# Optimization experiments

Measured on AMD Instinct MI355X. Metric: run time of the kernel, lower is better.

Reference implementation:

```python
import jax, jax.numpy as jnp
import numpy as np

FEAT_STRIDE = 16
PRE_NMS = 6000   # TEST config
POST_NMS = 300
NMS_TH = 0.7


def _generate_anchors_3d(base_size=16, ratios=(0.5, 1.0, 2.0), scales=(8, 16, 32), time_dims=(16,)):
    """Standard Faster-RCNN anchor enumeration, extended with a time extent.
    Returns (A, 6) float32 boxes in [x1, y1, z1, x2, y2, z2] order (matches shift order)."""
    w = h = float(base_size)
    xc = yc = 0.5 * (base_size - 1)
    size = w * h
    ratios = np.asarray(ratios, dtype=np.float64)
    ws = np.round(np.sqrt(size / ratios))
    hs = np.round(ws * ratios)
    a2 = []
    for wi, hi in zip(ws, hs):
        for s in scales:
            ww, hh = wi * s, hi * s
            a2.append([xc - 0.5 * (ww - 1), yc - 0.5 * (hh - 1),
                       xc + 0.5 * (ww - 1), yc + 0.5 * (hh - 1)])
    out = []
    for t in time_dims:
        for a in a2:
            out.append([a[0], a[1], 0.0, a[2], a[3], float(t) - 1.0])
    return np.asarray(out, dtype=np.float32)


def setup_inputs() -> dict:
    key = jax.random.key(0)
    k1, k2 = jax.random.split(key)
    B, A, H, W, T = 2, 9, 32, 32, 16
    scores_map = jax.random.normal(k1, (B, 2 * A, H, W, T), dtype=jnp.float32)
    bbox_frame = jax.random.normal(k2, (B, 6 * A, H, W, T), dtype=jnp.float32) * 0.2
    im_info = jnp.array([512.0, 512.0, 16.0], dtype=jnp.float32)  # [img_h, img_w, n_frames]
    anchors = jnp.asarray(_generate_anchors_3d())  # (9, 6)
    return {"scores_map": scores_map, "bbox_frame": bbox_frame, "im_info": im_info, "anchors": anchors}


def _nms_single(boxes, scs):
    """Greedy 3D (spatio-temporal volume) NMS for one image.
    boxes: (N, 6), scs: (N,). Returns (POST_NMS, 7) rows [score, x1,y1,z1,x2,y2,z2],
    zero-padded past the number of kept proposals (matches output[i].zero_() + fill)."""
    order = jnp.argsort(-scs)[:PRE_NMS]           # descending score, pre-NMS top-k
    b = boxes[order]                              # (P, 6)
    s = scs[order]                                # (P,)
    vol = (b[:, 3] - b[:, 0] + 1.0) * (b[:, 4] - b[:, 1] + 1.0) * (b[:, 5] - b[:, 2] + 1.0)
    iw = jnp.clip(jnp.minimum(b[:, None, 3], b[None, :, 3]) - jnp.maximum(b[:, None, 0], b[None, :, 0]) + 1.0, 0.0)
    ih = jnp.clip(jnp.minimum(b[:, None, 4], b[None, :, 4]) - jnp.maximum(b[:, None, 1], b[None, :, 1]) + 1.0, 0.0)
    il = jnp.clip(jnp.minimum(b[:, None, 5], b[None, :, 5]) - jnp.maximum(b[:, None, 2], b[None, :, 2]) + 1.0, 0.0)
    inter = iw * ih * il                          # (P, P)
    iou = inter / (vol[:, None] + vol[None, :] - inter)
    iou = jax.lax.stop_gradient(iou)              # keep mask is non-differentiable
    P = b.shape[0]
    idx = jnp.arange(P)

    def step(keep, i):
        sup = (iou[i] > NMS_TH) & keep[i] & (idx > i)
        return keep & ~sup, None

    keep, _ = jax.lax.scan(step, jnp.ones((P,), dtype=bool), jnp.arange(P))
    rank = jnp.cumsum(keep) - 1
    pos = jnp.where(keep & (rank < POST_NMS), rank, POST_NMS)  # overflow slot POST_NMS
    rows = jnp.concatenate([s[:, None], b], axis=1)            # (P, 7)
    out = jnp.zeros((POST_NMS + 1, 7), dtype=boxes.dtype).at[pos].set(rows)
    return out[:POST_NMS]


def reference(scores_map, bbox_frame, im_info, anchors):
    A = anchors.shape[0]
    B = scores_map.shape[0]
    scores = scores_map[:, A:]                    # (B, A, H, W, T) foreground scores
    H, W, T = scores.shape[2], scores.shape[3], scores.shape[4]

    # --- anchor grid (matches np.meshgrid 'xy' + ravel = H-major, W, T order) ---
    sx = (jnp.arange(W) * FEAT_STRIDE).astype(scores_map.dtype)
    sy = (jnp.arange(H) * FEAT_STRIDE).astype(scores_map.dtype)
    sz = jnp.arange(T).astype(scores_map.dtype)
    X, Y, Z = jnp.meshgrid(sx, sy, sz)            # each (H, W, T)
    shift = jnp.stack([X.ravel(), Y.ravel(), Z.ravel()], axis=1)   # (K, 3)
    shifts = jnp.concatenate([shift, shift], axis=1)               # (K, 6)
    all_anchors = (anchors[None] + shifts[:, None]).reshape(-1, 6)  # (K*A, 6)

    deltas = bbox_frame.transpose(0, 2, 3, 4, 1).reshape(B, -1, 6)  # (B, K*A, 6)
    scs = scores.transpose(0, 2, 3, 4, 1).reshape(B, -1)            # (B, K*A)

    # --- bbox_transform_inv_3d ---
    aw = all_anchors[:, 3] - all_anchors[:, 0] + 1.0
    ah = all_anchors[:, 4] - all_anchors[:, 1] + 1.0
    al = all_anchors[:, 5] - all_anchors[:, 2] + 1.0
    acx = all_anchors[:, 0] + 0.5 * aw
    acy = all_anchors[:, 1] + 0.5 * ah
    acz = all_anchors[:, 2] + 0.5 * al
    pcx = deltas[..., 0] * aw + acx
    pcy = deltas[..., 1] * ah + acy
    pcz = deltas[..., 2] * al + acz
    pw = jnp.exp(deltas[..., 3]) * aw
    ph = jnp.exp(deltas[..., 4]) * ah
    pl = jnp.exp(deltas[..., 5]) * al
    proposals = jnp.stack([pcx - 0.5 * pw, pcy - 0.5 * ph, pcz - 0.5 * pl,
                           pcx + 0.5 * pw, pcy + 0.5 * ph, pcz + 0.5 * pl], axis=-1)

    # --- clip_boxes_3d: x in [0, img_w-1], y in [0, img_h-1], z in [0, n_frames-1] ---
    lim = jnp.stack([im_info[1], im_info[0], im_info[2],
                     im_info[1], im_info[0], im_info[2]]) - 1.0
    proposals = jnp.clip(proposals, 0.0, lim)

    return jax.vmap(_nms_single)(proposals, scs)  # (B, POST_NMS, 7)
```

## Files before the change

### kernel.cpp

```cpp
#include <hip/hip_runtime.h>
#include <stdint.h>

#define FEAT_STRIDE 16
#define PRE_NMS 6000
#define POST_NMS 300
#define NMS_TH 0.7f

static constexpr int B_ = 2, A_ = 9, H_ = 32, W_ = 32, T_ = 16;
static constexpr int LOC = H_ * W_ * T_;
static constexpr int N_ = LOC * A_;
static constexpr int NBIN = 65536;
static constexpr int NREP = 8;
static constexpr int CAP = 8192;
static constexpr int NW = 94;
static constexpr int ROWS = 6016;


__device__ __forceinline__ uint32_t f2u(float f) {
    uint32_t b = __float_as_uint(f);
    return b ^ ((b >> 31) ? 0xFFFFFFFFu : 0x80000000u);
}
__device__ __forceinline__ float u2f(uint32_t u) {
    uint32_t b = (u >> 31) ? (u ^ 0x80000000u) : ~u;
    return __uint_as_float(b);
}

__global__ void hist_kernel(const float* __restrict__ scores_map,
                            unsigned int* __restrict__ histR) {
    int gid = blockIdx.x * blockDim.x + threadIdx.x;
    if (gid >= B_ * N_) return;
    int b = gid / N_;
    int r = gid - b * N_;
    int a = r / LOC;
    int loc = r - a * LOC;
    float sc = scores_map[((size_t)(b * 2 * A_ + A_ + a)) * LOC + loc];
    uint32_t u = f2u(sc);
    int rep = blockIdx.x & (NREP - 1);
    atomicAdd(&histR[((size_t)(rep * B_ + b)) * NBIN + (u >> 16)], 1u);
}

__global__ void __launch_bounds__(256) partial_kernel(
        const unsigned int* __restrict__ histR,
        unsigned int* __restrict__ partials) {
    int c = blockIdx.x, bb = blockIdx.y, t = threadIdx.x;
    unsigned int s = 0;
#pragma unroll
    for (int r = 0; r < NREP; ++r) {
        const uint4* h4 = reinterpret_cast<const uint4*>(
            histR + ((size_t)(r * B_ + bb)) * NBIN + c * 1024);
        uint4 v = h4[t];
        s += v.x + v.y + v.z + v.w;
    }
    __shared__ unsigned int red[256];
    red[t] = s;
    __syncthreads();
    for (int off = 128; off > 0; off >>= 1) {
        if (t < off) red[t] += red[t + off];
        __syncthreads();
    }
    if (t == 0) partials[bb * 64 + c] = red[0];
}

__global__ void __launch_bounds__(256) rewrite_kernel(
        const unsigned int* __restrict__ histR,
        unsigned int* __restrict__ hist,
        unsigned int* __restrict__ binbase,
        const unsigned int* __restrict__ partials,
        unsigned int* __restrict__ thr) {
    int c = blockIdx.x, bb = blockIdx.y, t = threadIdx.x;
    __shared__ unsigned int sp[64];
    __shared__ unsigned int ssum[256];
    if (t < 64) sp[t] = partials[bb * 64 + t];
    uint4 v = {0u, 0u, 0u, 0u};
#pragma unroll
    for (int r = 0; r < NREP; ++r) {
        const uint4* h4 = reinterpret_cast<const uint4*>(
            histR + ((size_t)(r * B_ + bb)) * NBIN + c * 1024);
        uint4 w = h4[t];
        v.x += w.x; v.y += w.y; v.z += w.z; v.w += w.w;
    }
    unsigned int* h = hist + (size_t)bb * NBIN + c * 1024;
    unsigned int* bs = binbase + (size_t)bb * NBIN + c * 1024;
    ssum[t] = v.x + v.y + v.z + v.w;
    __syncthreads();
    unsigned int chunkBase = 0;
    for (int q = c + 1; q < 64; ++q) chunkBase += sp[q];
    for (int off = 1; off < 256; off <<= 1) {
        unsigned int val = (t + off < 256) ? ssum[t + off] : 0u;
        __syncthreads();
        ssum[t] += val;
        __syncthreads();
    }
    unsigned int run = chunkBase + ((t < 255) ? ssum[t + 1] : 0u);
    unsigned int cnt[4] = {v.x, v.y, v.z, v.w};
    unsigned int offv[4];
    for (int q = 3; q >= 0; --q) {
        offv[q] = run;
        unsigned int newrun = run + cnt[q];
        if (run < (unsigned)PRE_NMS && newrun >= (unsigned)PRE_NMS) {
            thr[bb * 2 + 0] = (unsigned)(c * 1024 + t * 4 + q);
            thr[bb * 2 + 1] = newrun;
        }
        run = newrun;
    }
    uint4 o4 = {offv[0], offv[1], offv[2], offv[3]};
    reinterpret_cast<uint4*>(h)[t] = o4;
    reinterpret_cast<uint4*>(bs)[t] = o4;
}

__global__ void __launch_bounds__(256) compact_kernel(
        const float* __restrict__ scores_map,
        const unsigned int* __restrict__ thr,
        unsigned long long* __restrict__ cand,
        unsigned int* __restrict__ hist) {
    int tid = threadIdx.x;
    int gid = blockIdx.x * 256 + tid;
    int b = gid / N_;
    int r = gid - b * N_;
    int a = r / LOC;
    int loc = r - a * LOC;
    float sc = scores_map[((size_t)(b * 2 * A_ + A_ + a)) * LOC + loc];
    uint32_t u = f2u(sc);
    uint32_t bin = u >> 16;
    if (bin >= thr[b * 2]) {
        int n = loc * A_ + a;
        unsigned long long key = ((unsigned long long)u << 18)
                               | (unsigned long long)(N_ - 1 - n);
        unsigned int slot = atomicAdd(&hist[b * NBIN + bin], 1u);
        if (slot < (unsigned)CAP)
            cand[(size_t)b * CAP + slot] = key;
    }
}

__global__ void __launch_bounds__(256) bucket_decode(
        const unsigned long long* __restrict__ cand,
        const unsigned int* __restrict__ hist,
        const unsigned int* __restrict__ binbase,
        const unsigned int* __restrict__ thr,
        const float* __restrict__ bbox_frame,
        const float* __restrict__ im_info,
        const float* __restrict__ anchors,
        float* __restrict__ sortedBox) {
    int gid = blockIdx.x * 256 + threadIdx.x;
    int bb = gid / CAP;
    int i = gid - bb * CAP;
    int count = (int)thr[bb * 2 + 1];
    if (count > CAP) count = CAP;
    if (i >= count) return;
    const unsigned long long* cb = cand + (size_t)bb * CAP;
    unsigned long long me = cb[i];
    int bin = (int)(me >> 34);
    int start = (int)binbase[bb * NBIN + bin];
    int end = (int)hist[bb * NBIN + bin];
    if (end > count) end = count;
    int rank = start;
    for (int q = start; q < end; ++q)
        rank += (cb[q] > me);
    if (rank >= PRE_NMS) return;

    uint32_t u = (uint32_t)(me >> 18);
    int n = N_ - 1 - (int)(me & 0x3FFFFull);
    int a = n % A_;
    int loc = n / A_;
    int k = loc % T_;
    int j = (loc / T_) % W_;
    int ii = loc / (T_ * W_);

    float ax1 = anchors[a * 6 + 0] + (float)(FEAT_STRIDE * j);
    float ay1 = anchors[a * 6 + 1] + (float)(FEAT_STRIDE * ii);
    float az1 = anchors[a * 6 + 2] + (float)k;
    float ax2 = anchors[a * 6 + 3] + (float)(FEAT_STRIDE * j);
    float ay2 = anchors[a * 6 + 4] + (float)(FEAT_STRIDE * ii);
    float az2 = anchors[a * 6 + 5] + (float)k;
    float aw = ax2 - ax1 + 1.0f, ah = ay2 - ay1 + 1.0f, al = az2 - az1 + 1.0f;
    float acx = ax1 + 0.5f * aw, acy = ay1 + 0.5f * ah, acz = az1 + 0.5f * al;

    const float* dp = bbox_frame + ((size_t)(bb * 6 * A_ + a * 6)) * LOC
                    + ii * (W_ * T_) + j * T_ + k;
    float d0 = dp[0 * LOC], d1 = dp[1 * LOC], d2 = dp[2 * LOC];
    float d3 = dp[3 * LOC], d4 = dp[4 * LOC], d5 = dp[5 * LOC];

    float pcx = d0 * aw + acx, pcy = d1 * ah + acy, pcz = d2 * al + acz;
    float pw = expf(d3) * aw, ph = expf(d4) * ah, pl = expf(d5) * al;

    float x1 = pcx - 0.5f * pw, y1 = pcy - 0.5f * ph, z1 = pcz - 0.5f * pl;
    float x2 = pcx + 0.5f * pw, y2 = pcy + 0.5f * ph, z2 = pcz + 0.5f * pl;

    float lx = im_info[1] - 1.0f, ly = im_info[0] - 1.0f, lz = im_info[2] - 1.0f;
    x1 = fminf(fmaxf(x1, 0.0f), lx); y1 = fminf(fmaxf(y1, 0.0f), ly); z1 = fminf(fmaxf(z1, 0.0f), lz);
    x2 = fminf(fmaxf(x2, 0.0f), lx); y2 = fminf(fmaxf(y2, 0.0f), ly); z2 = fminf(fmaxf(z2, 0.0f), lz);

    float vol = (x2 - x1 + 1.0f) * (y2 - y1 + 1.0f) * (z2 - z1 + 1.0f);
    float* p = sortedBox + ((size_t)bb * ROWS + rank) * 8;
    p[0] = x1; p[1] = y1; p[2] = z1; p[3] = x2;
    p[4] = y2; p[5] = z2; p[6] = vol; p[7] = u2f(u);
}

__global__ void mask_build(const float* __restrict__ sortedBox,
                           unsigned long long* __restrict__ mask,
                           unsigned long long* __restrict__ diagBand) {
    int g = blockIdx.x / NW, w = blockIdx.x % NW;
    if (w < g) return;
    int bb = blockIdx.y;
    int lane = threadIdx.x;
    __shared__ float colb[64][7];
    const float* sb = sortedBox + (size_t)bb * ROWS * 8;
    int col = w * 64 + lane;
    if (col < PRE_NMS) {
        const float4* cp4 = reinterpret_cast<const float4*>(sb + (size_t)col * 8);
        float4 lo = cp4[0], hi = cp4[1];
        colb[lane][0] = lo.x; colb[lane][1] = lo.y; colb[lane][2] = lo.z;
        colb[lane][3] = lo.w; colb[lane][4] = hi.x; colb[lane][5] = hi.y;
        colb[lane][6] = hi.z;
    } else {
        colb[lane][0] = 3e8f; colb[lane][1] = 0.f; colb[lane][2] = 0.f;
        colb[lane][3] = -3e8f; colb[lane][4] = 0.f; colb[lane][5] = 0.f;
        colb[lane][6] = 1.0f;
    }
    __syncthreads();
    int row = g * 64 + lane;
    if (row >= PRE_NMS) return;
    const float4* rp4 = reinterpret_cast<const float4*>(sb + (size_t)row * 8);
    float4 rlo = rp4[0], rhi = rp4[1];
    float x1 = rlo.x, y1 = rlo.y, z1 = rlo.z;
    float x2 = rlo.w, y2 = rhi.x, z2 = rhi.y, v = rhi.z;
    unsigned long long word = 0;
    for (int b2 = 0; b2 < 64; ++b2) {
        float iw = fminf(x2, colb[b2][3]) - fmaxf(x1, colb[b2][0]) + 1.0f;
        float ih = fminf(y2, colb[b2][4]) - fmaxf(y1, colb[b2][1]) + 1.0f;
        float il = fminf(z2, colb[b2][5]) - fmaxf(z1, colb[b2][2]) + 1.0f;
        iw = fmaxf(iw, 0.0f); ih = fmaxf(ih, 0.0f); il = fmaxf(il, 0.0f);
        float inter = iw * ih * il;
        float iou = inter / (v + colb[b2][6] - inter);
        int cidx = w * 64 + b2;
        if (cidx > row && iou > NMS_TH) word |= (1ull << b2);
    }
    mask[((size_t)bb * ROWS + row) * NW + w] = word;
    if (w == g) {
        diagBand[((size_t)bb * ROWS + row) * 2 + 0] = word;
        if (g == NW - 1) diagBand[((size_t)bb * ROWS + row) * 2 + 1] = 0ull;
    }
    if (w == g + 1) diagBand[((size_t)bb * ROWS + row) * 2 + 1] = word;
}

__global__ void __launch_bounds__(1024) suppress_kernel(
        const unsigned long long* __restrict__ mask,
        const unsigned long long* __restrict__ diagBand,
        const float* __restrict__ sortedBox,
        float* __restrict__ out) {
    int bb = blockIdx.x;
    int tid = threadIdx.x;
    int lane = tid & 63;
    __shared__ unsigned long long remv[NW];
    __shared__ int kr[2][64];
    __shared__ int s_nk;
    for (int i = tid; i < NW; i += 1024) remv[i] = 0ull;
    if (tid == 0) {
        remv[NW - 1] = ~((1ull << (PRE_NMS - (NW - 1) * 64)) - 1ull);
        s_nk = 0;
    }
    __syncthreads();

    const unsigned long long* M = mask + (size_t)bb * ROWS * NW;
    const unsigned long long* D = diagBand + (size_t)bb * ROWS * 2;
    const float* sb = sortedBox + (size_t)bb * ROWS * 8;
    float* ob = out + (size_t)bb * POST_NMS * 7;

    int kept_total = 0, prev_nk = 0, prev_base = 0, cur = 0;
    unsigned long long diag0 = 0, band1 = 0, sup = 0;
    if (tid < 64) {
        diag0 = D[lane * 2 + 0];
        band1 = D[lane * 2 + 1];
    }

    for (int c = 0; c < NW; ++c) {
        unsigned long long nxt0 = 0, nxt1 = 0;
        if (tid < 64) {
            if (c + 1 < NW) {
                nxt0 = D[((c + 1) * 64 + lane) * 2 + 0];
                nxt1 = D[((c + 1) * 64 + lane) * 2 + 1];
            }
            unsigned long long alive = ~(remv[c] | sup);
            unsigned long long supn = 0;
            int nk = 0;
            while (alive && kept_total + nk < POST_NMS) {
                int b = __builtin_ctzll(alive);
                if (lane == 0) kr[cur][nk] = c * 64 + b;
                ++nk;
                alive &= ~(__shfl(diag0, b) | (1ull << b));
                supn |= __shfl(band1, b);
            }
            sup = supn;
            if (tid == 0) s_nk = nk;
        } else {
            int t = tid - 64;
            for (int w2 = c + 1 + t; w2 < NW; w2 += 960) {
                unsigned long long v = remv[w2];
                for (int i = 0; i < prev_nk; ++i)
                    v |= M[(size_t)kr[cur ^ 1][i] * NW + w2];
                remv[w2] = v;
            }
            for (int e = t; e < prev_nk * 7; e += 960) {
                int i = e / 7, j = e - i * 7;
                ob[(size_t)(prev_base + i) * 7 + j] =
                    sb[(size_t)kr[cur ^ 1][i] * 8 + (j == 0 ? 7 : j - 1)];
            }
        }
        __syncthreads();
        int nk = s_nk;
        prev_base = kept_total;
        kept_total += nk;
        prev_nk = nk;
        cur ^= 1;
        if (tid < 64) { diag0 = nxt0; band1 = nxt1; }
        if (kept_total >= POST_NMS) break;
    }
    for (int e = tid; e < prev_nk * 7; e += 1024) {
        int i = e / 7, j = e - i * 7;
        ob[(size_t)(prev_base + i) * 7 + j] =
            sb[(size_t)kr[cur ^ 1][i] * 8 + (j == 0 ? 7 : j - 1)];
    }
    for (int idx = kept_total * 7 + tid; idx < POST_NMS * 7; idx += 1024)
        ob[idx] = 0.0f;
}

extern "C" void kernel_launch(void* const* d_in, const int* in_sizes, int n_in,
                              void* d_out, int out_size, void* d_ws, size_t ws_size,
                              hipStream_t stream) {
    const float* scores_map = (const float*)d_in[0];
    const float* bbox_frame = (const float*)d_in[1];
    const float* im_info    = (const float*)d_in[2];
    const float* anchors    = (const float*)d_in[3];
    float* out = (float*)d_out;

    char* ws = (char*)d_ws;
    unsigned long long* mask     = (unsigned long long*)(ws + 0);
    unsigned int* binbase        = (unsigned int*)(ws + 0);
    unsigned int* histR          = (unsigned int*)(ws + 524288);
    float* sortedBox             = (float*)(ws + 9048064);
    unsigned long long* cand     = (unsigned long long*)(ws + 9433088);
    unsigned int* hist           = (unsigned int*)(ws + 9564160);
    unsigned long long* diagBand = (unsigned long long*)(ws + 9564160);
    unsigned int* thr            = (unsigned int*)(ws + 10088448);
    unsigned int* partials       = (unsigned int*)(ws + 10088464);

    hipMemsetAsync(histR, 0, (size_t)NREP * B_ * NBIN * 4, stream);

    int total = B_ * N_;
    hist_kernel<<<(total + 255) / 256, 256, 0, stream>>>(scores_map, histR);
    partial_kernel<<<dim3(64, B_), 256, 0, stream>>>(histR, partials);
    rewrite_kernel<<<dim3(64, B_), 256, 0, stream>>>(histR, hist, binbase, partials, thr);
    compact_kernel<<<total / 256, 256, 0, stream>>>(scores_map, thr, cand, hist);
    bucket_decode<<<B_ * CAP / 256, 256, 0, stream>>>(cand, hist, binbase, thr,
                                                      bbox_frame, im_info, anchors,
                                                      sortedBox);
    mask_build<<<dim3(NW * NW, B_), 64, 0, stream>>>(sortedBox, mask, diagBand);
    suppress_kernel<<<B_, 1024, 0, stream>>>(mask, diagBand, sortedBox, out);
}
```

Baseline: 144.3 us.

## Replace IoU division with double-precision compare, vectorize shared column loads, transpose mask

The per-pair IoU division in mask building is replaced by a multiply-compare in double against a constant chosen to reproduce the float `iou > 0.7` decision. Column boxes are staged in shared memory as two float4 arrays so each inner iteration does vector LDS reads, and the loop is unrolled. The suppression mask is stored word-major instead of row-major, so the suppress kernel reads one mask word's rows at contiguous addresses. Double-precision arithmetic may be slower on some paths, and the exactness of the threshold equivalence depends on the chosen constant.

New measurement: 134.1 us. 1.08x faster.

```diff
diff --git a/kernel.cpp b/kernel.cpp
--- a/kernel.cpp
+++ b/kernel.cpp
@@ -14,6 +14,8 @@
 static constexpr int CAP = 8192;
 static constexpr int NW = 94;
 static constexpr int ROWS = 6016;
+
+static constexpr double BMID = 0.7000000178813934326171875;
 
 
 __device__ __forceinline__ uint32_t f2u(float f) {
@@ -203,19 +205,18 @@
     if (w < g) return;
     int bb = blockIdx.y;
     int lane = threadIdx.x;
-    __shared__ float colb[64][7];
+    __shared__ float4 colA[64];
+    __shared__ float4 colB[64];
     const float* sb = sortedBox + (size_t)bb * ROWS * 8;
     int col = w * 64 + lane;
     if (col < PRE_NMS) {
         const float4* cp4 = reinterpret_cast<const float4*>(sb + (size_t)col * 8);
         float4 lo = cp4[0], hi = cp4[1];
-        colb[lane][0] = lo.x; colb[lane][1] = lo.y; colb[lane][2] = lo.z;
-        colb[lane][3] = lo.w; colb[lane][4] = hi.x; colb[lane][5] = hi.y;
-        colb[lane][6] = hi.z;
+        colA[lane] = make_float4(lo.x, lo.y, lo.z, lo.w);
+        colB[lane] = make_float4(hi.x, hi.y, hi.z, 0.0f);
     } else {
-        colb[lane][0] = 3e8f; colb[lane][1] = 0.f; colb[lane][2] = 0.f;
-        colb[lane][3] = -3e8f; colb[lane][4] = 0.f; colb[lane][5] = 0.f;
-        colb[lane][6] = 1.0f;
+        colA[lane] = make_float4(3e8f, 0.0f, 0.0f, -3e8f);
+        colB[lane] = make_float4(0.0f, 0.0f, 1.0f, 0.0f);
     }
     __syncthreads();
     int row = g * 64 + lane;
@@ -225,17 +226,21 @@
     float x1 = rlo.x, y1 = rlo.y, z1 = rlo.z;
     float x2 = rlo.w, y2 = rhi.x, z2 = rhi.y, v = rhi.z;
     unsigned long long word = 0;
+#pragma unroll 8
     for (int b2 = 0; b2 < 64; ++b2) {
-        float iw = fminf(x2, colb[b2][3]) - fmaxf(x1, colb[b2][0]) + 1.0f;
-        float ih = fminf(y2, colb[b2][4]) - fmaxf(y1, colb[b2][1]) + 1.0f;
-        float il = fminf(z2, colb[b2][5]) - fmaxf(z1, colb[b2][2]) + 1.0f;
+        float4 cA = colA[b2];
+        float4 cB = colB[b2];
+        float iw = fminf(x2, cA.w) - fmaxf(x1, cA.x) + 1.0f;
+        float ih = fminf(y2, cB.x) - fmaxf(y1, cA.y) + 1.0f;
+        float il = fminf(z2, cB.y) - fmaxf(z1, cA.z) + 1.0f;
         iw = fmaxf(iw, 0.0f); ih = fmaxf(ih, 0.0f); il = fmaxf(il, 0.0f);
         float inter = iw * ih * il;
-        float iou = inter / (v + colb[b2][6] - inter);
+        float denom = v + cB.z - inter;
+        bool over = ((double)inter >= BMID * (double)denom);
         int cidx = w * 64 + b2;
-        if (cidx > row && iou > NMS_TH) word |= (1ull << b2);
-    }
-    mask[((size_t)bb * ROWS + row) * NW + w] = word;
+        if (cidx > row && over) word |= (1ull << b2);
+    }
+    mask[((size_t)bb * NW + w) * ROWS + row] = word;
     if (w == g) {
         diagBand[((size_t)bb * ROWS + row) * 2 + 0] = word;
         if (g == NW - 1) diagBand[((size_t)bb * ROWS + row) * 2 + 1] = 0ull;
@@ -261,7 +266,7 @@
     }
     __syncthreads();
 
-    const unsigned long long* M = mask + (size_t)bb * ROWS * NW;
+    const unsigned long long* M = mask + (size_t)bb * NW * ROWS;
     const unsigned long long* D = diagBand + (size_t)bb * ROWS * 2;
     const float* sb = sortedBox + (size_t)bb * ROWS * 8;
     float* ob = out + (size_t)bb * POST_NMS * 7;
@@ -295,10 +300,10 @@
         } else {
             int t = tid - 64;
             for (int w2 = c + 1 + t; w2 < NW; w2 += 960) {
-                unsigned long long v = remv[w2];
+                unsigned long long vv = remv[w2];
                 for (int i = 0; i < prev_nk; ++i)
-                    v |= M[(size_t)kr[cur ^ 1][i] * NW + w2];
-                remv[w2] = v;
+                    vv |= M[(size_t)w2 * ROWS + kr[cur ^ 1][i]];
+                remv[w2] = vv;
             }
             for (int e = t; e < prev_nk * 7; e += 960) {
                 int i = e / 7, j = e - i * 7;
```
